# Kernel tuning notes

Measured on AMD Instinct MI355X. Metric: run time of the kernel, lower is better.

Reference implementation:

```python
import jax, jax.numpy as jnp
import numpy as np

N_HEADS = 16
LN_EPS = 1e-5


def _layer_norm(x, g, b):
    mu = jnp.mean(x, axis=-1, keepdims=True)
    var = jnp.mean(jnp.square(x - mu), axis=-1, keepdims=True)
    return (x - mu) * jax.lax.rsqrt(var + LN_EPS) * g + b


def setup_inputs() -> dict:
    key = jax.random.key(0)
    ks = jax.random.split(key, 6)
    B, S, D = 2, 2048, 1024
    d_ff = 4 * D
    sc = lambda fan_in: 1.0 / np.sqrt(fan_in)
    return {
        "x": jax.random.normal(ks[0], (B, S, D), jnp.float32),
        "in_proj_w": jax.random.normal(ks[1], (3 * D, D), jnp.float32) * sc(D),
        "in_proj_b": jnp.zeros((3 * D,), jnp.float32),
        "out_proj_w": jax.random.normal(ks[2], (D, D), jnp.float32) * sc(D),
        "out_proj_b": jnp.zeros((D,), jnp.float32),
        "ln1_g": jnp.ones((D,), jnp.float32),
        "ln1_b": jnp.zeros((D,), jnp.float32),
        "w1": jax.random.normal(ks[3], (d_ff, D), jnp.float32) * sc(D),
        "b1": jnp.zeros((d_ff,), jnp.float32),
        "w2": jax.random.normal(ks[4], (D, d_ff), jnp.float32) * sc(d_ff),
        "b2": jnp.zeros((D,), jnp.float32),
        "ln2_g": jnp.ones((D,), jnp.float32),
        "ln2_b": jnp.zeros((D,), jnp.float32),
        "window": 128,
    }


def reference(x, in_proj_w, in_proj_b, out_proj_w, out_proj_b,
              ln1_g, ln1_b, w1, b1, w2, b2, ln2_g, ln2_b, window):
    B, S, D = x.shape
    H = N_HEADS
    hd = D // H

    # fused QKV projection (torch Linear convention: x @ W.T + b)
    qkv = x @ in_proj_w.T + in_proj_b            # (B, S, 3D)
    q, k, v = jnp.split(qkv, 3, axis=-1)
    to_heads = lambda t: t.reshape(B, S, H, hd).transpose(0, 2, 1, 3)  # (B,H,S,hd)
    q, k, v = to_heads(q), to_heads(k), to_heads(v)

    scores = jnp.einsum("bhqd,bhkd->bhqk", q, k) / jnp.sqrt(jnp.asarray(hd, x.dtype))
    # banded mask: position i attends to j with |i - j| <= window
    idx = jnp.arange(S)
    band = jnp.abs(idx[:, None] - idx[None, :]) <= window   # (S, S) bool
    scores = jnp.where(band, scores, -jnp.inf)
    probs = jax.nn.softmax(scores, axis=-1)

    attn = jnp.einsum("bhqk,bhkd->bhqd", probs, v)           # (B,H,S,hd)
    attn = attn.transpose(0, 2, 1, 3).reshape(B, S, D)
    attn_out = attn @ out_proj_w.T + out_proj_b

    x2 = _layer_norm(x + attn_out, ln1_g, ln1_b)
    ff = jax.nn.relu(x2 @ w1.T + b1) @ w2.T + b2
    x3 = _layer_norm(x2 + ff, ln2_g, ln2_b)
    return x3
```

## Files before the change

kernel.cpp:

```cpp
#include <hip/hip_runtime.h>
#include <hip/hip_bf16.h>

#define AS1 __attribute__((address_space(1)))
#define AS3 __attribute__((address_space(3)))

typedef __bf16 bf16x8_t __attribute__((ext_vector_type(8)));
typedef float f32x4_t __attribute__((ext_vector_type(4)));
typedef unsigned short ushort_t;
typedef unsigned int uint_t;

static __device__ __forceinline__ ushort_t f2b(float f) {
    __hip_bfloat16 h = __float2bfloat16(f);
    return __builtin_bit_cast(unsigned short, h);
}

struct CastArgs {
    const float* src[5];
    ushort_t* dst[5];
    int cum[6];
};

__global__ __launch_bounds__(256) void cast_all(CastArgs a) {
    const int i = blockIdx.x * 256 + threadIdx.x;
    if (i >= a.cum[5]) return;
    int s = 0;
#pragma unroll
    for (int k = 1; k < 5; ++k) s += (i >= a.cum[k]);
    const int idx = i - a.cum[s];
    float4 v = ((const float4*)a.src[s])[idx];
    ushort4 o;
    o.x = f2b(v.x); o.y = f2b(v.y); o.z = f2b(v.z); o.w = f2b(v.w);
    ((ushort4*)a.dst[s])[idx] = o;
}

#define EPI_BIAS 1
#define EPI_RELU 2
#define EPI_OUTF 8
#define EPI_OUTB 16

struct P4 { float* p[4]; };

template <int F>
__global__ __launch_bounds__(256, 2) void gemm_bt(const ushort_t* __restrict__ A,
                                                  const ushort_t* __restrict__ B,
                                                  const float* __restrict__ bias,
                                                  P4 outs,
                                                  ushort_t* __restrict__ outb,
                                                  int M, int N, int Kc, int ld) {
    __shared__ ushort_t la[128 * 32];
    __shared__ ushort_t lb[128 * 32];
    const int t = threadIdx.x;
    const int n0 = blockIdx.x * 128;
    const int m0 = blockIdx.y * 128;
    const int z = blockIdx.z;
    const int k0 = z * Kc;
    const int lane = t & 63;
    const int w = t >> 6;
    const int wr = w >> 1, wc = w & 1;
    const int r16 = lane & 15, kq = lane >> 4;

    const int srow = t >> 2;
    const int scg = t & 3;

    f32x4_t acc[4][4] = {};

    const size_t arow0 = (size_t)(m0 + srow) * ld + scg * 8 + k0;
    const size_t brow0 = (size_t)(n0 + srow) * ld + scg * 8 + k0;

    for (int kk = 0; kk < Kc; kk += 32) {
#pragma unroll
        for (int p = 0; p < 2; ++p) {
            const ushort_t* ga = A + arow0 + (size_t)p * 64 * ld + kk;
            const ushort_t* gb = B + brow0 + (size_t)p * 64 * ld + kk;
            __builtin_amdgcn_global_load_lds((AS1 void*)ga, (AS3 void*)(la + (t + 256 * p) * 8), 16, 0, 0);
            __builtin_amdgcn_global_load_lds((AS1 void*)gb, (AS3 void*)(lb + (t + 256 * p) * 8), 16, 0, 0);
        }
        __syncthreads();
        bf16x8_t af[4], bfr[4];
#pragma unroll
        for (int mi = 0; mi < 4; ++mi)
            af[mi] = *(const bf16x8_t*)(la + (wr * 64 + mi * 16 + r16) * 32 + kq * 8);
#pragma unroll
        for (int ni = 0; ni < 4; ++ni)
            bfr[ni] = *(const bf16x8_t*)(lb + (wc * 64 + ni * 16 + r16) * 32 + kq * 8);
#pragma unroll
        for (int mi = 0; mi < 4; ++mi)
#pragma unroll
            for (int ni = 0; ni < 4; ++ni)
                acc[mi][ni] = __builtin_amdgcn_mfma_f32_16x16x32_bf16(af[mi], bfr[ni], acc[mi][ni], 0, 0, 0);
        __syncthreads();
    }

    float* outf = outs.p[z];
#pragma unroll
    for (int mi = 0; mi < 4; ++mi) {
#pragma unroll
        for (int ni = 0; ni < 4; ++ni) {
            const int row = m0 + wr * 64 + mi * 16 + kq * 4;
            const int col = n0 + wc * 64 + ni * 16 + r16;
            float bv = (F & EPI_BIAS) ? bias[col] : 0.f;
#pragma unroll
            for (int i = 0; i < 4; ++i) {
                float v = acc[mi][ni][i] + bv;
                const size_t off = (size_t)(row + i) * N + col;
                if (F & EPI_RELU) v = fmaxf(v, 0.f);
                if (F & EPI_OUTF) outf[off] = v;
                if (F & EPI_OUTB) outb[off] = f2b(v);
            }
        }
    }
}

__global__ __launch_bounds__(256, 4) void flash_mfma(const ushort_t* __restrict__ qkv,
                                                     ushort_t* __restrict__ attn) {
    const int S = 2048;
    const int h = blockIdx.y, bb = blockIdx.z;
    const int q0 = blockIdx.x * 64;
    const int t = threadIdx.x;
    const int w = t >> 6, lane = t & 63;
    const int r16 = lane & 15, g = lane >> 4;

    __shared__ ushort_t lk[64 * 72];
    __shared__ ushort_t lv[64 * 68];
    __shared__ ushort_t lp[4 * 16 * 72];

    const ushort_t* base = qkv + (size_t)bb * S * 3072 + (size_t)h * 64;

    bf16x8_t qa[2];
    {
        const ushort_t* qrow = base + (size_t)(q0 + 16 * w + r16) * 3072;
        qa[0] = *(const bf16x8_t*)(qrow + g * 8);
        qa[1] = *(const bf16x8_t*)(qrow + 32 + g * 8);
    }

    f32x4_t O[4] = {};
    float mrow[4] = {-1e30f, -1e30f, -1e30f, -1e30f};
    float lrow[4] = {0.f, 0.f, 0.f, 0.f};

    for (int it = 0; it < 5; ++it) {
        const int kt0 = q0 - 128 + 64 * it;
        if (kt0 < 0 || kt0 >= S) continue;

#pragma unroll
        for (int pass = 0; pass < 2; ++pass) {
            const int c = t + 256 * pass;
            const int key = c >> 3, dc = c & 7;
            const ushort_t* src = base + (size_t)(kt0 + key) * 3072 + dc * 8;
            uint4 kk = *(const uint4*)(src + 1024);
            uint4 vv = *(const uint4*)(src + 2048);
            *(uint4*)(lk + key * 72 + dc * 8) = kk;
            uint2* vd = (uint2*)(lv + key * 68 + dc * 8);
            vd[0] = make_uint2(vv.x, vv.y);
            vd[1] = make_uint2(vv.z, vv.w);
        }
        __syncthreads();

        f32x4_t s[4];
#pragma unroll
        for (int sub = 0; sub < 4; ++sub) {
            const ushort_t* krow = lk + (16 * sub + r16) * 72;
            bf16x8_t kb0 = *(const bf16x8_t*)(krow + g * 8);
            bf16x8_t kb1 = *(const bf16x8_t*)(krow + 32 + g * 8);
            f32x4_t z = {};
            z = __builtin_amdgcn_mfma_f32_16x16x32_bf16(qa[0], kb0, z, 0, 0, 0);
            z = __builtin_amdgcn_mfma_f32_16x16x32_bf16(qa[1], kb1, z, 0, 0, 0);
            s[sub] = z;
        }

        float alpha[4];
#pragma unroll
        for (int reg = 0; reg < 4; ++reg) {
            const int i = q0 + 16 * w + g * 4 + reg;
            float rm = -1e30f;
#pragma unroll
            for (int sub = 0; sub < 4; ++sub) {
                const int j = kt0 + 16 * sub + r16;
                const int d = i - j;
                const bool valid = (d <= 128) && (d >= -128);
                float v = valid ? s[sub][reg] * 0.125f : -1e30f;
                s[sub][reg] = v;
                rm = fmaxf(rm, v);
            }
#pragma unroll
            for (int msk = 1; msk < 16; msk <<= 1) rm = fmaxf(rm, __shfl_xor(rm, msk));
            const float mnew = fmaxf(mrow[reg], rm);
            alpha[reg] = __expf(mrow[reg] - mnew);
            mrow[reg] = mnew;
            float rs = 0.f;
#pragma unroll
            for (int sub = 0; sub < 4; ++sub) {
                float p = __expf(s[sub][reg] - mnew);
                s[sub][reg] = p;
                rs += p;
            }
#pragma unroll
            for (int msk = 1; msk < 16; msk <<= 1) rs += __shfl_xor(rs, msk);
            lrow[reg] = lrow[reg] * alpha[reg] + rs;
#pragma unroll
            for (int dd = 0; dd < 4; ++dd) O[dd][reg] *= alpha[reg];
        }

        ushort_t* pw = lp + w * 16 * 72;
#pragma unroll
        for (int sub = 0; sub < 4; ++sub)
#pragma unroll
            for (int reg = 0; reg < 4; ++reg)
                pw[(g * 4 + reg) * 72 + 16 * sub + r16] = f2b(s[sub][reg]);

        bf16x8_t pa0 = *(const bf16x8_t*)(pw + r16 * 72 + g * 8);
        bf16x8_t pa1 = *(const bf16x8_t*)(pw + r16 * 72 + 32 + g * 8);
        const __bf16* lvb = (const __bf16*)lv;
#pragma unroll
        for (int dd = 0; dd < 4; ++dd) {
            bf16x8_t vb0, vb1;
#pragma unroll
            for (int j = 0; j < 8; ++j) {
                vb0[j] = lvb[(g * 8 + j) * 68 + dd * 16 + r16];
                vb1[j] = lvb[(32 + g * 8 + j) * 68 + dd * 16 + r16];
            }
            O[dd] = __builtin_amdgcn_mfma_f32_16x16x32_bf16(pa0, vb0, O[dd], 0, 0, 0);
            O[dd] = __builtin_amdgcn_mfma_f32_16x16x32_bf16(pa1, vb1, O[dd], 0, 0, 0);
        }
        __syncthreads();
    }

#pragma unroll
    for (int reg = 0; reg < 4; ++reg) {
        const float inv = 1.0f / lrow[reg];
        const int i = q0 + 16 * w + g * 4 + reg;
        ushort_t* orow = attn + ((size_t)(bb * S + i)) * 1024 + (size_t)h * 64;
#pragma unroll
        for (int dd = 0; dd < 4; ++dd)
            orow[dd * 16 + r16] = f2b(O[dd][reg] * inv);
    }
}

template <int NP>
__global__ __launch_bounds__(256) void ln_red(const float* __restrict__ p0,
                                              const float* __restrict__ p1,
                                              const float* __restrict__ p2,
                                              const float* __restrict__ p3,
                                              const float* __restrict__ bias,
                                              const float* __restrict__ res,
                                              const float* __restrict__ g,
                                              const float* __restrict__ bta,
                                              float* __restrict__ outf,
                                              ushort_t* __restrict__ outb) {
    const int row = blockIdx.x;
    const int t = threadIdx.x;
    const size_t idx = (size_t)row * 256 + t;
    float4 v = ((const float4*)p0)[idx];
    {
        float4 a = ((const float4*)p1)[idx];
        v.x += a.x; v.y += a.y; v.z += a.z; v.w += a.w;
    }
    if (NP == 4) {
        float4 a = ((const float4*)p2)[idx];
        float4 b = ((const float4*)p3)[idx];
        v.x += a.x + b.x; v.y += a.y + b.y; v.z += a.z + b.z; v.w += a.w + b.w;
    }
    {
        float4 bb = ((const float4*)bias)[t];
        float4 rr = ((const float4*)res)[idx];
        v.x += bb.x + rr.x; v.y += bb.y + rr.y; v.z += bb.z + rr.z; v.w += bb.w + rr.w;
    }

    float s = v.x + v.y + v.z + v.w;
    float s2 = v.x * v.x + v.y * v.y + v.z * v.z + v.w * v.w;
#pragma unroll
    for (int off = 32; off > 0; off >>= 1) {
        s += __shfl_down(s, off);
        s2 += __shfl_down(s2, off);
    }
    __shared__ float red[8];
    const int w = t >> 6, lane = t & 63;
    if (lane == 0) { red[w] = s; red[4 + w] = s2; }
    __syncthreads();
    float S1 = red[0] + red[1] + red[2] + red[3];
    float S2 = red[4] + red[5] + red[6] + red[7];
    float mean = S1 * (1.f / 1024.f);
    float var = S2 * (1.f / 1024.f) - mean * mean;
    float r = rsqrtf(var + 1e-5f);
    float4 gg = ((const float4*)g)[t];
    float4 bb = ((const float4*)bta)[t];
    float4 o;
    o.x = (v.x - mean) * r * gg.x + bb.x;
    o.y = (v.y - mean) * r * gg.y + bb.y;
    o.z = (v.z - mean) * r * gg.z + bb.z;
    o.w = (v.w - mean) * r * gg.w + bb.w;
    ((float4*)outf)[idx] = o;
    if (outb) {
        ushort4 ob;
        ob.x = f2b(o.x); ob.y = f2b(o.y); ob.z = f2b(o.z); ob.w = f2b(o.w);
        ((ushort4*)outb)[idx] = ob;
    }
}

extern "C" void kernel_launch(void* const* d_in, const int* in_sizes, int n_in,
                              void* d_out, int out_size, void* d_ws, size_t ws_size,
                              hipStream_t stream) {
    const float* x          = (const float*)d_in[0];
    const float* in_proj_w  = (const float*)d_in[1];
    const float* in_proj_b  = (const float*)d_in[2];
    const float* out_proj_w = (const float*)d_in[3];
    const float* out_proj_b = (const float*)d_in[4];
    const float* ln1_g      = (const float*)d_in[5];
    const float* ln1_b      = (const float*)d_in[6];
    const float* w1         = (const float*)d_in[7];
    const float* b1         = (const float*)d_in[8];
    const float* w2         = (const float*)d_in[9];
    const float* b2         = (const float*)d_in[10];
    const float* ln2_g      = (const float*)d_in[11];
    const float* ln2_b      = (const float*)d_in[12];

    char* ws = (char*)d_ws;
    ushort_t* xb    = (ushort_t*)(ws + (0ull << 20));
    ushort_t* wqkvb = (ushort_t*)(ws + (8ull << 20));
    ushort_t* woutb = (ushort_t*)(ws + (14ull << 20));
    ushort_t* w1b   = (ushort_t*)(ws + (16ull << 20));
    ushort_t* w2b   = (ushort_t*)(ws + (24ull << 20));
    ushort_t* qkvb  = (ushort_t*)(ws + (32ull << 20));
    ushort_t* attnb = (ushort_t*)(ws + (56ull << 20));
    float*    y1    = (float*)(ws + (64ull << 20));
    float*    x2f   = (float*)(ws + (80ull << 20));
    ushort_t* x2b   = (ushort_t*)(ws + (96ull << 20));
    ushort_t* hb    = (ushort_t*)(ws + (104ull << 20));
    float* op_p1  = (float*)(ws + (32ull << 20));
    float* f2_p1  = (float*)(ws + (0ull << 20));
    float* f2_p2  = (float*)(ws + (32ull << 20));
    float* f2_p3  = (float*)(ws + (48ull << 20));
    (void)in_sizes; (void)n_in; (void)out_size; (void)ws_size;

    CastArgs ca;
    ca.src[0] = x;  ca.dst[0] = xb;
    ca.src[1] = in_proj_w;  ca.dst[1] = wqkvb;
    ca.src[2] = out_proj_w; ca.dst[2] = woutb;
    ca.src[3] = w1; ca.dst[3] = w1b;
    ca.src[4] = w2; ca.dst[4] = w2b;
    ca.cum[0] = 0;
    ca.cum[1] = 1048576;
    ca.cum[2] = 1048576 + 786432;
    ca.cum[3] = 1048576 + 786432 + 262144;
    ca.cum[4] = 1048576 + 786432 + 262144 + 1048576;
    ca.cum[5] = 1048576 + 786432 + 262144 + 1048576 + 1048576;
    cast_all<<<(ca.cum[5] + 255) / 256, 256, 0, stream>>>(ca);

    P4 none = {{nullptr, nullptr, nullptr, nullptr}};

    gemm_bt<EPI_BIAS | EPI_OUTB><<<dim3(24, 32, 1), 256, 0, stream>>>(
        xb, wqkvb, in_proj_b, none, qkvb, 4096, 3072, 1024, 1024);

    flash_mfma<<<dim3(32, 16, 2), 256, 0, stream>>>(qkvb, attnb);

    P4 op = {{y1, op_p1, nullptr, nullptr}};
    gemm_bt<EPI_OUTF><<<dim3(8, 32, 2), 256, 0, stream>>>(
        attnb, woutb, nullptr, op, nullptr, 4096, 1024, 512, 1024);

    ln_red<2><<<4096, 256, 0, stream>>>(y1, op_p1, nullptr, nullptr,
                                        out_proj_b, x, ln1_g, ln1_b, x2f, x2b);

    gemm_bt<EPI_BIAS | EPI_RELU | EPI_OUTB><<<dim3(32, 32, 1), 256, 0, stream>>>(
        x2b, w1b, b1, none, hb, 4096, 4096, 1024, 1024);

    P4 f2 = {{y1, f2_p1, f2_p2, f2_p3}};
    gemm_bt<EPI_OUTF><<<dim3(8, 32, 4), 256, 0, stream>>>(
        hb, w2b, nullptr, f2, nullptr, 4096, 1024, 1024, 4096);

    ln_red<4><<<4096, 256, 0, stream>>>(y1, f2_p1, f2_p2, f2_p3,
                                        b2, x2f, ln2_g, ln2_b, (float*)d_out, nullptr);
}
```

Before: 337.2 us.

## Store split-K partials in bf16 and remap GEMM blocks per XCD

Split-K partial sums of the output-projection and FFN2 GEMMs are now written as bf16 instead of fp32, and the LayerNorm reduction kernels read and widen them. This halves the partial-sum write and read traffic. Block indices are also remapped so each XCD works on a contiguous band of M rows, which should improve L2 reuse of the A tiles. The cost is extra rounding error in the partials before the residual add and LayerNorm.

```diff
diff --git a/kernel.cpp b/kernel.cpp
--- a/kernel.cpp
+++ b/kernel.cpp
@@ -12,6 +12,9 @@
 static __device__ __forceinline__ ushort_t f2b(float f) {
     __hip_bfloat16 h = __float2bfloat16(f);
     return __builtin_bit_cast(unsigned short, h);
+}
+static __device__ __forceinline__ float b2f(ushort_t u) {
+    return __uint_as_float((uint_t)u << 16);
 }
 
 struct CastArgs {
@@ -35,24 +38,33 @@
 
 #define EPI_BIAS 1
 #define EPI_RELU 2
-#define EPI_OUTF 8
+#define EPI_PART 8
 #define EPI_OUTB 16
 
-struct P4 { float* p[4]; };
+struct PB { ushort_t* p[4]; };
 
 template <int F>
 __global__ __launch_bounds__(256, 2) void gemm_bt(const ushort_t* __restrict__ A,
                                                   const ushort_t* __restrict__ B,
                                                   const float* __restrict__ bias,
-                                                  P4 outs,
+                                                  PB pb,
                                                   ushort_t* __restrict__ outb,
                                                   int M, int N, int Kc, int ld) {
     __shared__ ushort_t la[128 * 32];
     __shared__ ushort_t lb[128 * 32];
     const int t = threadIdx.x;
-    const int n0 = blockIdx.x * 128;
-    const int m0 = blockIdx.y * 128;
-    const int z = blockIdx.z;
+
+    const int nx = gridDim.x, ny = gridDim.y, nz = gridDim.z;
+    const int lid = blockIdx.x + nx * (blockIdx.y + ny * blockIdx.z);
+    const int xcd = lid & 7;
+    const int slot = lid >> 3;
+    const int n_i = slot % nx;
+    const int rest = slot / nx;
+    const int z = rest % nz;
+    const int m_i = xcd * (ny >> 3) + rest / nz;
+
+    const int n0 = n_i * 128;
+    const int m0 = m_i * 128;
     const int k0 = z * Kc;
     const int lane = t & 63;
     const int w = t >> 6;
@@ -91,7 +103,7 @@
         __syncthreads();
     }
 
-    float* outf = outs.p[z];
+    ushort_t* po = (F & EPI_PART) ? pb.p[z] : outb;
 #pragma unroll
     for (int mi = 0; mi < 4; ++mi) {
 #pragma unroll
@@ -104,8 +116,7 @@
                 float v = acc[mi][ni][i] + bv;
                 const size_t off = (size_t)(row + i) * N + col;
                 if (F & EPI_RELU) v = fmaxf(v, 0.f);
-                if (F & EPI_OUTF) outf[off] = v;
-                if (F & EPI_OUTB) outb[off] = f2b(v);
+                po[off] = f2b(v);
             }
         }
     }
@@ -236,10 +247,10 @@
 }
 
 template <int NP>
-__global__ __launch_bounds__(256) void ln_red(const float* __restrict__ p0,
-                                              const float* __restrict__ p1,
-                                              const float* __restrict__ p2,
-                                              const float* __restrict__ p3,
+__global__ __launch_bounds__(256) void ln_red(const ushort_t* __restrict__ p0,
+                                              const ushort_t* __restrict__ p1,
+                                              const ushort_t* __restrict__ p2,
+                                              const ushort_t* __restrict__ p3,
                                               const float* __restrict__ bias,
                                               const float* __restrict__ res,
                                               const float* __restrict__ g,
@@ -249,15 +260,22 @@
     const int row = blockIdx.x;
     const int t = threadIdx.x;
     const size_t idx = (size_t)row * 256 + t;
-    float4 v = ((const float4*)p0)[idx];
+    float4 v;
     {
-        float4 a = ((const float4*)p1)[idx];
-        v.x += a.x; v.y += a.y; v.z += a.z; v.w += a.w;
+        ushort4 a = ((const ushort4*)p0)[idx];
+        ushort4 b = ((const ushort4*)p1)[idx];
+        v.x = b2f(a.x) + b2f(b.x);
+        v.y = b2f(a.y) + b2f(b.y);
+        v.z = b2f(a.z) + b2f(b.z);
+        v.w = b2f(a.w) + b2f(b.w);
     }
     if (NP == 4) {
-        float4 a = ((const float4*)p2)[idx];
-        float4 b = ((const float4*)p3)[idx];
-        v.x += a.x + b.x; v.y += a.y + b.y; v.z += a.z + b.z; v.w += a.w + b.w;
+        ushort4 a = ((const ushort4*)p2)[idx];
+        ushort4 b = ((const ushort4*)p3)[idx];
+        v.x += b2f(a.x) + b2f(b.x);
+        v.y += b2f(a.y) + b2f(b.y);
+        v.z += b2f(a.z) + b2f(b.z);
+        v.w += b2f(a.w) + b2f(b.w);
     }
     {
         float4 bb = ((const float4*)bias)[t];
@@ -321,14 +339,15 @@
     ushort_t* w2b   = (ushort_t*)(ws + (24ull << 20));
     ushort_t* qkvb  = (ushort_t*)(ws + (32ull << 20));
     ushort_t* attnb = (ushort_t*)(ws + (56ull << 20));
-    float*    y1    = (float*)(ws + (64ull << 20));
     float*    x2f   = (float*)(ws + (80ull << 20));
     ushort_t* x2b   = (ushort_t*)(ws + (96ull << 20));
     ushort_t* hb    = (ushort_t*)(ws + (104ull << 20));
-    float* op_p1  = (float*)(ws + (32ull << 20));
-    float* f2_p1  = (float*)(ws + (0ull << 20));
-    float* f2_p2  = (float*)(ws + (32ull << 20));
-    float* f2_p3  = (float*)(ws + (48ull << 20));
+    ushort_t* op_p0 = (ushort_t*)(ws + (64ull << 20));
+    ushort_t* op_p1 = (ushort_t*)(ws + (72ull << 20));
+    ushort_t* f2_p0 = (ushort_t*)(ws + (0ull << 20));
+    ushort_t* f2_p1 = (ushort_t*)(ws + (8ull << 20));
+    ushort_t* f2_p2 = (ushort_t*)(ws + (32ull << 20));
+    ushort_t* f2_p3 = (ushort_t*)(ws + (40ull << 20));
     (void)in_sizes; (void)n_in; (void)out_size; (void)ws_size;
 
     CastArgs ca;
@@ -345,27 +364,27 @@
     ca.cum[5] = 1048576 + 786432 + 262144 + 1048576 + 1048576;
     cast_all<<<(ca.cum[5] + 255) / 256, 256, 0, stream>>>(ca);
 
-    P4 none = {{nullptr, nullptr, nullptr, nullptr}};
+    PB none = {{nullptr, nullptr, nullptr, nullptr}};
 
     gemm_bt<EPI_BIAS | EPI_OUTB><<<dim3(24, 32, 1), 256, 0, stream>>>(
         xb, wqkvb, in_proj_b, none, qkvb, 4096, 3072, 1024, 1024);
 
     flash_mfma<<<dim3(32, 16, 2), 256, 0, stream>>>(qkvb, attnb);
 
-    P4 op = {{y1, op_p1, nullptr, nullptr}};
-    gemm_bt<EPI_OUTF><<<dim3(8, 32, 2), 256, 0, stream>>>(
+    PB op = {{op_p0, op_p1, nullptr, nullptr}};
+    gemm_bt<EPI_PART><<<dim3(8, 32, 2), 256, 0, stream>>>(
         attnb, woutb, nullptr, op, nullptr, 4096, 1024, 512, 1024);
 
-    ln_red<2><<<4096, 256, 0, stream>>>(y1, op_p1, nullptr, nullptr,
+    ln_red<2><<<4096, 256, 0, stream>>>(op_p0, op_p1, nullptr, nullptr,
                                         out_proj_b, x, ln1_g, ln1_b, x2f, x2b);
 
     gemm_bt<EPI_BIAS | EPI_RELU | EPI_OUTB><<<dim3(32, 32, 1), 256, 0, stream>>>(
         x2b, w1b, b1, none, hb, 4096, 4096, 1024, 1024);
 
-    P4 f2 = {{y1, f2_p1, f2_p2, f2_p3}};
-    gemm_bt<EPI_OUTF><<<dim3(8, 32, 4), 256, 0, stream>>>(
+    PB f2 = {{f2_p0, f2_p1, f2_p2, f2_p3}};
+    gemm_bt<EPI_PART><<<dim3(8, 32, 4), 256, 0, stream>>>(
         hb, w2b, nullptr, f2, nullptr, 4096, 1024, 1024, 4096);
 
-    ln_red<4><<<4096, 256, 0, stream>>>(y1, f2_p1, f2_p2, f2_p3,
+    ln_red<4><<<4096, 256, 0, stream>>>(f2_p0, f2_p1, f2_p2, f2_p3,
                                         b2, x2f, ln2_g, ln2_b, (float*)d_out, nullptr);
 }
```

After: 312.1 us. 1.08x faster.
